# Optimization experiments

Measured on AMD Instinct MI355X. Metric: run time of the kernel, lower is better.

## Reference

```python
import jax, jax.numpy as jnp
import numpy as np

SIGMA_E, SIGMA_I, K_E, K_I = 0.6, 1.2, 0.8, 1.0
PM_STEPS, DT, BETA = 4, 0.15, 1.0
EPS = 1e-4


def setup_inputs() -> dict:
    key = jax.random.key(0)
    ks = jax.random.split(key, 12)
    B, d_in, d_lat, ch, d_out, n_c = 4096, 784, 8, 32, 10, 16
    inp = {
        "x": jax.random.normal(ks[0], (B, d_in), dtype=jnp.float32),
        "W1": jax.random.normal(ks[1], (d_in, 128), dtype=jnp.float32) * 0.03,
        "b1": jnp.zeros((128,), jnp.float32),
        "W2": jax.random.normal(ks[2], (128, d_lat), dtype=jnp.float32) * 0.08,
        "b2": jnp.zeros((d_lat,), jnp.float32),
        "centers": jax.random.normal(ks[3], (n_c, d_lat), dtype=jnp.float32) * 0.7,
        "mus": jnp.ones((n_c,), jnp.float32) * 0.5,
        "Wp": jax.random.normal(ks[4], (d_lat, ch), dtype=jnp.float32) * 0.3,
        "bp": jnp.zeros((ch,), jnp.float32),
        "Wr": jax.random.normal(ks[5], (ch, d_out), dtype=jnp.float32) * 0.15,
        "br": jnp.zeros((d_out,), jnp.float32),
        "T": 5,
    }
    return inp


def grad_ln_n(z, centers, mus):
    # z: [B,d], centers: [C,d], mus: [C]
    rvec = z[:, None, :] - centers[None, :, :]          # [B,C,d]
    r = jnp.sqrt(jnp.sum(rvec * rvec, axis=-1) + EPS)   # [B,C]
    n = 1.0 + jnp.sum(mus[None, :] / r, axis=1)          # [B]
    g = -jnp.sum((mus[None, :] / (r ** 3))[:, :, None] * rvec, axis=1)  # [B,d]
    return g / n[:, None]


def pm_field(z, centers, mus):
    for _ in range(PM_STEPS):
        z = jnp.clip(z + DT * BETA * grad_ln_n(z, centers, mus), -3.0, 3.0)
    return z


def lateral_kernel(z):
    # squared pairwise distances via the norm trick (avoids [B,B,d])
    sq = jnp.sum(z * z, axis=1)
    dist2 = jnp.maximum(sq[:, None] + sq[None, :] - 2.0 * (z @ z.T), 0.0)
    K = K_E * jnp.exp(-dist2 / (2.0 * SIGMA_E ** 2)) - K_I * jnp.exp(-dist2 / (2.0 * SIGMA_I ** 2))
    return jax.lax.stop_gradient(K)  # torch.no_grad in original


def reference(x, W1, b1, W2, b2, centers, mus, Wp, bp, Wr, br, T):
    B = x.shape[0]
    z = jnp.tanh(x.reshape(B, -1) @ W1 + b1) @ W2 + b2   # encoder
    h = jnp.zeros((B, Wr.shape[0]), x.dtype)
    for _ in range(T):
        z = pm_field(z, centers, mus)
        h = 0.9 * h + 0.1 * jnp.tanh(z @ Wp + bp)
        h = h + 0.05 * (lateral_kernel(z) @ h)
        y = h @ Wr + br
    return y
```

## Files before the change

kernel.cpp:

```cpp
#include <hip/hip_runtime.h>
#include <math.h>

#define NB    4096
#define DIN   784
#define DH    128
#define DL    8
#define NC    16
#define NCH   32
#define DO    10
#define TSTEPS 5

#define KH_ROWS   128
#define KH_JSLICE 128
#define KH_P      (NB / KH_JSLICE)
#define ENC_G     7

typedef float v2f __attribute__((ext_vector_type(2)));


__global__ __launch_bounds__(256) void enc1_kernel(const float* __restrict__ x,
    const float* __restrict__ W1, double* __restrict__ P)
{
    __shared__ float xsT[56][18];
    __shared__ float wss[56][128];
    const int tid = threadIdx.x;
    const int m0 = blockIdx.x * 16;
    const int kbeg = blockIdx.y * 112;
    const int cg = tid & 31, rg = tid >> 5;
    const int c0 = cg << 2, r0 = rg << 1;
    double acc[2][4] = {};
    for (int it = 0; it < 2; ++it) {
        const int k0 = kbeg + it * 56;
        __syncthreads();
        if (tid < 224) {
            int row = tid / 14, f = tid % 14;
            float4 v = *(const float4*)(x + (m0 + row) * DIN + k0 + f * 4);
            int kk = f * 4;
            xsT[kk][row] = v.x; xsT[kk + 1][row] = v.y;
            xsT[kk + 2][row] = v.z; xsT[kk + 3][row] = v.w;
        }
        for (int l = tid; l < 56 * 32; l += 256) {
            int kk = l >> 5, c = (l & 31) << 2;
            *(float4*)&wss[kk][c] = *(const float4*)(W1 + (k0 + kk) * DH + c);
        }
        __syncthreads();
#pragma unroll 8
        for (int kk = 0; kk < 56; ++kk) {
            const float2 xv = *(const float2*)&xsT[kk][r0];
            const float4 wv = *(const float4*)&wss[kk][c0];
            const double x0 = (double)xv.x, x1 = (double)xv.y;
            const double w0 = (double)wv.x, w1 = (double)wv.y;
            const double w2v = (double)wv.z, w3 = (double)wv.w;
            acc[0][0] += x0 * w0; acc[0][1] += x0 * w1;
            acc[0][2] += x0 * w2v; acc[0][3] += x0 * w3;
            acc[1][0] += x1 * w0; acc[1][1] += x1 * w1;
            acc[1][2] += x1 * w2v; acc[1][3] += x1 * w3;
        }
    }
    double* Pr = P + (size_t)blockIdx.y * (NB * DH);
#pragma unroll
    for (int i = 0; i < 2; ++i) {
        double* dst = Pr + (m0 + r0 + i) * DH + c0;
        *(double2*)dst       = make_double2(acc[i][0], acc[i][1]);
        *(double2*)(dst + 2) = make_double2(acc[i][2], acc[i][3]);
    }
}

__global__ __launch_bounds__(256) void enc2_kernel(const double* __restrict__ P,
    const float* __restrict__ b1, const float* __restrict__ W2,
    const float* __restrict__ b2, double* __restrict__ zbuf)
{
    __shared__ double As[16][132];
    __shared__ double W2d[DH * DL];
    const int tid = threadIdx.x;
    const int m0 = blockIdx.x * 16;
    for (int l = tid; l < DH * DL; l += 256) W2d[l] = (double)W2[l];
    for (int l = tid; l < 16 * 128; l += 256) {
        int row = l >> 7, k = l & 127;
        double v = (double)b1[k];
#pragma unroll
        for (int s = 0; s < ENC_G; ++s)
            v += P[(size_t)s * NB * DH + (m0 + row) * DH + k];
        As[row][k] = tanh(v);
    }
    __syncthreads();
    const int row = tid >> 4, d = (tid >> 1) & 7, half = tid & 1;
    double a = 0.0;
#pragma unroll 8
    for (int i = 0; i < 64; ++i) {
        const int k = half + (i << 1);
        a += As[row][k] * W2d[k * 8 + d];
    }
    a += __shfl_xor(a, 1);
    if (half == 0) zbuf[(m0 + row) * DL + d] = a + (double)b2[d];
}

__global__ __launch_bounds__(256) void enc_fused_kernel(const float* __restrict__ x,
    const float* __restrict__ W1, const float* __restrict__ b1,
    const float* __restrict__ W2, const float* __restrict__ b2,
    double* __restrict__ zbuf)
{
    __shared__ float  xsT[56][9];
    __shared__ float  wss[56][128];
    __shared__ double Asd[8][131];
    __shared__ double W2d[DH * DL];
    const int tid = threadIdx.x;
    const int m0 = blockIdx.x * 8;
    const int cg = tid & 31, rg = tid >> 5;
    const int c0 = cg << 2;
    for (int l = tid; l < DH * DL; l += 256) W2d[l] = (double)W2[l];
    double acc[4] = {};
    for (int it = 0; it < 14; ++it) {
        const int k0 = it * 56;
        __syncthreads();
        if (tid < 112) {
            int row = tid / 14, f = tid % 14;
            float4 v = *(const float4*)(x + (m0 + row) * DIN + k0 + f * 4);
            int kk = f * 4;
            xsT[kk][row] = v.x; xsT[kk + 1][row] = v.y;
            xsT[kk + 2][row] = v.z; xsT[kk + 3][row] = v.w;
        }
        for (int l = tid; l < 56 * 32; l += 256) {
            int kk = l >> 5, c = (l & 31) << 2;
            *(float4*)&wss[kk][c] = *(const float4*)(W1 + (k0 + kk) * DH + c);
        }
        __syncthreads();
#pragma unroll 8
        for (int kk = 0; kk < 56; ++kk) {
            const double xv = (double)xsT[kk][rg];
            const float4 wv = *(const float4*)&wss[kk][c0];
            acc[0] += xv * (double)wv.x;
            acc[1] += xv * (double)wv.y;
            acc[2] += xv * (double)wv.z;
            acc[3] += xv * (double)wv.w;
        }
    }
    __syncthreads();
#pragma unroll
    for (int j = 0; j < 4; ++j)
        Asd[rg][c0 + j] = tanh(acc[j] + (double)b1[c0 + j]);
    __syncthreads();
    {
        const int row = tid >> 5, d = (tid >> 2) & 7, kq = tid & 3;
        double a = 0.0;
#pragma unroll 8
        for (int i = 0; i < 32; ++i) {
            const int k = kq + (i << 2);
            a += Asd[row][k] * W2d[k * 8 + d];
        }
        a += __shfl_xor(a, 1);
        a += __shfl_xor(a, 2);
        if (kq == 0) zbuf[(m0 + row) * DL + d] = a + (double)b2[d];
    }
}

__global__ __launch_bounds__(64) void pmh_kernel(double* __restrict__ zbuf,
    const float* __restrict__ centers, const float* __restrict__ mus,
    const float* __restrict__ Wp, const float* __restrict__ bp,
    double* __restrict__ hB, float* __restrict__ zf, float* __restrict__ sqf,
    float* __restrict__ hAf, const float* __restrict__ part, int first)
{
    const int tid = threadIdx.x;
    const int lane = tid & 15;
    const int s = tid >> 4;
    const int i = blockIdx.x * 4 + s;
    double cz[8];
#pragma unroll
    for (int d = 0; d < 8; ++d) cz[d] = (double)centers[lane * DL + d];
    const double mu = (double)mus[lane];
    double z[8];
#pragma unroll
    for (int p = 0; p < 4; ++p) {
        double2 v = *(const double2*)(zbuf + i * DL + p * 2);
        z[p * 2] = v.x; z[p * 2 + 1] = v.y;
    }
#pragma unroll
    for (int st = 0; st < 4; ++st) {
        double rv[8];
        double ss = 1e-4;
#pragma unroll
        for (int d = 0; d < 8; ++d) { rv[d] = z[d] - cz[d]; ss += rv[d] * rv[d]; }
        double rinv = rsqrt(ss);
        double mr = mu * rinv;
        double n = mr;
        double mr3 = mr * (rinv * rinv);
        double g[8];
#pragma unroll
        for (int d = 0; d < 8; ++d) g[d] = -mr3 * rv[d];
#pragma unroll
        for (int m = 1; m < 16; m <<= 1) {
            n += __shfl_xor(n, m);
#pragma unroll
            for (int d = 0; d < 8; ++d) g[d] += __shfl_xor(g[d], m);
        }
        double sc = 0.15 / (1.0 + n);
#pragma unroll
        for (int d = 0; d < 8; ++d) z[d] = fmin(3.0, fmax(-3.0, z[d] + sc * g[d]));
    }
    if (lane == 0) {
        double sq = 0.0;
#pragma unroll
        for (int d = 0; d < 8; ++d) sq += z[d] * z[d];
        sqf[i] = (float)sq;
#pragma unroll
        for (int p = 0; p < 4; ++p)
            *(double2*)(zbuf + i * DL + p * 2) = make_double2(z[p * 2], z[p * 2 + 1]);
        float4 a = make_float4((float)z[0], (float)z[1], (float)z[2], (float)z[3]);
        float4 b = make_float4((float)z[4], (float)z[5], (float)z[6], (float)z[7]);
        *(float4*)(zf + i * DL)     = a;
        *(float4*)(zf + i * DL + 4) = b;
    }
#pragma unroll
    for (int cc = 0; cc < 2; ++cc) {
        const int c = lane + cc * 16;
        double a = (double)bp[c];
#pragma unroll
        for (int d = 0; d < 8; ++d) a += z[d] * (double)Wp[d * NCH + c];
        double ph = (double)tanhf((float)a);
        double prev = 0.0;
        if (!first) {
            prev = hB[i * NCH + c];
            if (part) {
                double sp = 0.0;
#pragma unroll
                for (int p = 0; p < KH_P; ++p)
                    sp += (double)part[(size_t)p * (NB * NCH) + i * NCH + c];
                prev += 0.05 * sp;
            }
        }
        double hv = 0.9 * prev + 0.1 * ph;
        hAf[i * NCH + c] = (float)hv;
        hB[i * NCH + c] = hv;
    }
}

#define SM_Z   0
#define SM_SQ  1024
#define SM_H   1152
#define SM_ALL 5248
__global__ __launch_bounds__(256) void kh_kernel(const float* __restrict__ zf,
    const float* __restrict__ sqf, const float* __restrict__ hAf,
    double* __restrict__ hB, float* __restrict__ part)
{
    __shared__ float smem[SM_ALL];
    const int tid = threadIdx.x;
    const int wave = tid >> 6, lane = tid & 63;
    const int row0 = blockIdx.x * KH_ROWS + lane;
    const int j0 = blockIdx.y * KH_JSLICE;
    float zr0[8], zr1[8];
    {
        float4 a = *(const float4*)(zf + row0 * 8);
        float4 b = *(const float4*)(zf + row0 * 8 + 4);
        zr0[0] = a.x; zr0[1] = a.y; zr0[2] = a.z; zr0[3] = a.w;
        zr0[4] = b.x; zr0[5] = b.y; zr0[6] = b.z; zr0[7] = b.w;
        float4 c = *(const float4*)(zf + (row0 + 64) * 8);
        float4 d = *(const float4*)(zf + (row0 + 64) * 8 + 4);
        zr1[0] = c.x; zr1[1] = c.y; zr1[2] = c.z; zr1[3] = c.w;
        zr1[4] = d.x; zr1[5] = d.y; zr1[6] = d.z; zr1[7] = d.w;
    }
    const float sq0 = sqf[row0], sq1 = sqf[row0 + 64];
    const float invI = 1.0f / 2.88f;
    {
        int jj = tid >> 1, p = (tid & 1) << 2;
        *(float4*)&smem[SM_Z + jj * 8 + p] = *(const float4*)(zf + (j0 + jj) * 8 + p);
    }
    if (tid < KH_JSLICE) smem[SM_SQ + tid] = sqf[j0 + tid];
    for (int l = tid; l < KH_JSLICE * 8; l += 256) {
        int jh = l >> 3, p = (l & 7) << 2;
        *(float4*)&smem[SM_H + jh * 32 + p] = *(const float4*)(hAf + (j0 + jh) * NCH + p);
    }
    __syncthreads();
    v2f a0[16], a1[16];
#pragma unroll
    for (int k = 0; k < 16; ++k) { a0[k] = (v2f)(0.f); a1[k] = (v2f)(0.f); }
    const int jjbeg = wave * 32;
#pragma unroll 2
    for (int q = 0; q < 32; ++q) {
        const int jj = jjbeg + q;
        const float4 a = *(const float4*)&smem[SM_Z + jj * 8];
        const float4 b = *(const float4*)&smem[SM_Z + jj * 8 + 4];
        const float sqj = smem[SM_SQ + jj];
        float dot0 = zr0[0] * a.x + zr0[1] * a.y + zr0[2] * a.z + zr0[3] * a.w
                   + zr0[4] * b.x + zr0[5] * b.y + zr0[6] * b.z + zr0[7] * b.w;
        float dot1 = zr1[0] * a.x + zr1[1] * a.y + zr1[2] * a.z + zr1[3] * a.w
                   + zr1[4] * b.x + zr1[5] * b.y + zr1[6] * b.z + zr1[7] * b.w;
        float d20 = fmaxf(sq0 + sqj - 2.0f * dot0, 0.0f);
        float d21 = fmaxf(sq1 + sqj - 2.0f * dot1, 0.0f);
        float e0 = __expf(-d20 * invI), e1 = __expf(-d21 * invI);
        float t0 = e0 * e0, t1 = e1 * e1;
        float K0 = 0.8f * (t0 * t0) - e0;
        float K1 = 0.8f * (t1 * t1) - e1;
        const v2f K0v = {K0, K0}, K1v = {K1, K1};
        const v2f* hrow = (const v2f*)&smem[SM_H + jj * 32];
#pragma unroll
        for (int k = 0; k < 16; k += 2) {
            const v2f h0 = hrow[k], h1 = hrow[k + 1];
            a0[k]     += K0v * h0; a0[k + 1] += K0v * h1;
            a1[k]     += K1v * h0; a1[k + 1] += K1v * h1;
        }
    }
    float* acc0 = (float*)a0;
    float* acc1 = (float*)a1;
    __syncthreads();
    if (wave == 1) {
#pragma unroll
        for (int c = 0; c < 32; ++c) { smem[lane * 33 + c] = acc0[c]; smem[(lane + 64) * 33 + c] = acc1[c]; }
    }
    __syncthreads();
    if (wave == 0) {
#pragma unroll
        for (int c = 0; c < 32; ++c) { acc0[c] += smem[lane * 33 + c]; acc1[c] += smem[(lane + 64) * 33 + c]; }
    }
    __syncthreads();
    if (wave == 3) {
#pragma unroll
        for (int c = 0; c < 32; ++c) { smem[lane * 33 + c] = acc0[c]; smem[(lane + 64) * 33 + c] = acc1[c]; }
    }
    __syncthreads();
    if (wave == 2) {
#pragma unroll
        for (int c = 0; c < 32; ++c) { acc0[c] += smem[lane * 33 + c]; acc1[c] += smem[(lane + 64) * 33 + c]; }
    }
    __syncthreads();
    if (wave == 2) {
#pragma unroll
        for (int c = 0; c < 32; ++c) { smem[lane * 33 + c] = acc0[c]; smem[(lane + 64) * 33 + c] = acc1[c]; }
    }
    __syncthreads();
    if (wave == 0) {
#pragma unroll
        for (int c = 0; c < 32; ++c) { acc0[c] += smem[lane * 33 + c]; acc1[c] += smem[(lane + 64) * 33 + c]; }
        if (part) {
            float* p0 = part + (size_t)blockIdx.y * (NB * NCH) + row0 * NCH;
            float* p1 = p0 + 64 * NCH;
#pragma unroll
            for (int c = 0; c < 32; c += 4) {
                *(float4*)(p0 + c) = make_float4(acc0[c], acc0[c + 1], acc0[c + 2], acc0[c + 3]);
                *(float4*)(p1 + c) = make_float4(acc1[c], acc1[c + 1], acc1[c + 2], acc1[c + 3]);
            }
        } else {
#pragma unroll
            for (int c = 0; c < 32; ++c) {
                atomicAdd(&hB[row0 * NCH + c], 0.05 * (double)acc0[c]);
                atomicAdd(&hB[(row0 + 64) * NCH + c], 0.05 * (double)acc1[c]);
            }
        }
    }
}

__global__ __launch_bounds__(256) void y_kernel(const double* __restrict__ h,
    const float* __restrict__ part, const float* __restrict__ Wr,
    const float* __restrict__ br, float* __restrict__ y)
{
    __shared__ double hsy[16][33];
    __shared__ double wrs[NCH * DO];
    __shared__ double brs[DO];
    const int tid = threadIdx.x;
    const int rb = blockIdx.x * 16;
    for (int l = tid; l < 16 * 32; l += 256) {
        int row = l >> 5, k = l & 31;
        const int gi = (rb + row) * NCH + k;
        double v = h[gi];
        if (part) {
            double sp = 0.0;
#pragma unroll
            for (int p = 0; p < KH_P; ++p) sp += (double)part[(size_t)p * (NB * NCH) + gi];
            v += 0.05 * sp;
        }
        hsy[row][k] = v;
    }
    for (int l = tid; l < NCH * DO; l += 256) wrs[l] = (double)Wr[l];
    if (tid < DO) brs[tid] = (double)br[tid];
    __syncthreads();
    const int row = tid >> 4, col = tid & 15;
    if (col < DO) {
        double a = brs[col];
#pragma unroll
        for (int k = 0; k < NCH; ++k) a += hsy[row][k] * wrs[k * DO + col];
        y[(rb + row) * DO + col] = (float)a;
    }
}

extern "C" void kernel_launch(void* const* d_in, const int* in_sizes, int n_in,
                              void* d_out, int out_size, void* d_ws, size_t ws_size,
                              hipStream_t stream)
{
    const float* x   = (const float*)d_in[0];
    const float* W1  = (const float*)d_in[1];
    const float* b1  = (const float*)d_in[2];
    const float* W2  = (const float*)d_in[3];
    const float* b2  = (const float*)d_in[4];
    const float* cen = (const float*)d_in[5];
    const float* mus = (const float*)d_in[6];
    const float* Wp  = (const float*)d_in[7];
    const float* bp  = (const float*)d_in[8];
    const float* Wr  = (const float*)d_in[9];
    const float* br  = (const float*)d_in[10];

    float* y = (float*)d_out;
    double* zbuf = (double*)d_ws;
    double* hB   = zbuf + NB * DL;
    float*  zf   = (float*)(hB + NB * NCH);
    float*  sqf  = zf + NB * DL;
    float*  hAf  = sqf + NB;
    float*  part = hAf + NB * NCH;
    double* Penc = (double*)(part + (size_t)KH_P * NB * NCH);

    const size_t need_part = (size_t)(NB * DL + NB * NCH) * 8
                           + (size_t)(NB * DL + NB + NB * NCH + KH_P * NB * NCH) * 4;
    const size_t need_full = need_part + (size_t)ENC_G * NB * DH * 8;
    float* pp = (ws_size >= need_part) ? part : (float*)nullptr;

    if (ws_size >= need_full) {
        enc1_kernel<<<dim3(NB / 16, ENC_G), 256, 0, stream>>>(x, W1, Penc);
        enc2_kernel<<<NB / 16, 256, 0, stream>>>(Penc, b1, W2, b2, zbuf);
    } else {
        enc_fused_kernel<<<NB / 8, 256, 0, stream>>>(x, W1, b1, W2, b2, zbuf);
    }
    for (int t = 0; t < TSTEPS; ++t) {
        pmh_kernel<<<NB / 4, 64, 0, stream>>>(zbuf, cen, mus, Wp, bp, hB,
                                              zf, sqf, hAf, pp, t == 0 ? 1 : 0);
        kh_kernel<<<dim3(NB / KH_ROWS, KH_P), 256, 0, stream>>>(zf, sqf, hAf, hB, pp);
    }
    y_kernel<<<NB / 16, 256, 0, stream>>>(hB, pp, Wr, br, y);
}
```

Before: 331.3 us.

## Fuse time-step loop into one persistent cooperative kernel with grid syncs

Replaces the 11 separate launches (pmh and kh kernels per step plus the y kernel) with a single cooperative persistent kernel. Blocks loop over virtual work items and use grid.sync between the PM/h phase and the lateral-kernel phase. This removes per-launch overhead and inter-kernel gaps, at the cost of grid-wide barriers and fewer resident blocks (grid capped at 1024) than the original launch sizes.

Measured after the change: 996.0 us. 3.01x slower.

```diff
diff --git a/kernel.cpp b/kernel.cpp
--- a/kernel.cpp
+++ b/kernel.cpp
@@ -1,4 +1,5 @@
 #include <hip/hip_runtime.h>
+#include <hip/hip_cooperative_groups.h>
 #include <math.h>
 
 #define NB    4096
@@ -154,6 +155,235 @@
     }
 }
 
+#define SM_Z   0
+#define SM_SQ  1024
+#define SM_H   1152
+#define SM_ALL 5248
+__global__ __launch_bounds__(256, 4) void loop_kernel(
+    double* __restrict__ zbuf, const float* __restrict__ cen,
+    const float* __restrict__ mus, const float* __restrict__ Wp,
+    const float* __restrict__ bp, double* __restrict__ hB,
+    float* __restrict__ zf, float* __restrict__ sqf, float* __restrict__ hAf,
+    float* __restrict__ part, const float* __restrict__ Wr,
+    const float* __restrict__ br, float* __restrict__ y)
+{
+    cooperative_groups::grid_group grid = cooperative_groups::this_grid();
+    __shared__ __align__(16) double dsm[2624];
+    float* smem = (float*)dsm;
+    const int tid = threadIdx.x;
+    const int nB = gridDim.x;
+
+    for (int t = 0; t < TSTEPS; ++t) {
+        {
+            const int wv = tid >> 6, wl = tid & 63;
+            const int l16 = wl & 15, sIdx = wl >> 4;
+            const int w = blockIdx.x * 4 + wv;
+            const int nW = nB * 4;
+            for (int g = w; g < NB / 4; g += nW) {
+                const int i = g * 4 + sIdx;
+                double cz[8];
+#pragma unroll
+                for (int d = 0; d < 8; ++d) cz[d] = (double)cen[l16 * DL + d];
+                const double mu = (double)mus[l16];
+                double z[8];
+#pragma unroll
+                for (int p = 0; p < 4; ++p) {
+                    double2 v = *(const double2*)(zbuf + i * DL + p * 2);
+                    z[p * 2] = v.x; z[p * 2 + 1] = v.y;
+                }
+#pragma unroll
+                for (int st = 0; st < 4; ++st) {
+                    double rv[8];
+                    double ss = 1e-4;
+#pragma unroll
+                    for (int d = 0; d < 8; ++d) { rv[d] = z[d] - cz[d]; ss += rv[d] * rv[d]; }
+                    double rinv = rsqrt(ss);
+                    double mr = mu * rinv;
+                    double n = mr;
+                    double mr3 = mr * (rinv * rinv);
+                    double gv[8];
+#pragma unroll
+                    for (int d = 0; d < 8; ++d) gv[d] = -mr3 * rv[d];
+#pragma unroll
+                    for (int m = 1; m < 16; m <<= 1) {
+                        n += __shfl_xor(n, m);
+#pragma unroll
+                        for (int d = 0; d < 8; ++d) gv[d] += __shfl_xor(gv[d], m);
+                    }
+                    double sc = 0.15 / (1.0 + n);
+#pragma unroll
+                    for (int d = 0; d < 8; ++d) z[d] = fmin(3.0, fmax(-3.0, z[d] + sc * gv[d]));
+                }
+                if (l16 == 0) {
+                    double sq = 0.0;
+#pragma unroll
+                    for (int d = 0; d < 8; ++d) sq += z[d] * z[d];
+                    sqf[i] = (float)sq;
+#pragma unroll
+                    for (int p = 0; p < 4; ++p)
+                        *(double2*)(zbuf + i * DL + p * 2) = make_double2(z[p * 2], z[p * 2 + 1]);
+                    float4 a = make_float4((float)z[0], (float)z[1], (float)z[2], (float)z[3]);
+                    float4 b = make_float4((float)z[4], (float)z[5], (float)z[6], (float)z[7]);
+                    *(float4*)(zf + i * DL)     = a;
+                    *(float4*)(zf + i * DL + 4) = b;
+                }
+#pragma unroll
+                for (int cc = 0; cc < 2; ++cc) {
+                    const int c = l16 + cc * 16;
+                    double a = (double)bp[c];
+#pragma unroll
+                    for (int d = 0; d < 8; ++d) a += z[d] * (double)Wp[d * NCH + c];
+                    double ph = (double)tanhf((float)a);
+                    double prev = 0.0;
+                    if (t != 0) {
+                        prev = hB[i * NCH + c];
+                        double sp = 0.0;
+#pragma unroll 8
+                        for (int p = 0; p < KH_P; ++p)
+                            sp += (double)part[(size_t)p * (NB * NCH) + i * NCH + c];
+                        prev += 0.05 * sp;
+                    }
+                    double hv = 0.9 * prev + 0.1 * ph;
+                    hAf[i * NCH + c] = (float)hv;
+                    hB[i * NCH + c] = hv;
+                }
+            }
+        }
+        grid.sync();
+        {
+            const int wave = tid >> 6, lane = tid & 63;
+            for (int vb = blockIdx.x; vb < (NB / KH_ROWS) * KH_P; vb += nB) {
+                const int bx = vb & (NB / KH_ROWS - 1);
+                const int by = vb / (NB / KH_ROWS);
+                __syncthreads();
+                const int row0 = bx * KH_ROWS + lane;
+                const int j0 = by * KH_JSLICE;
+                float zr0[8], zr1[8];
+                {
+                    float4 a = *(const float4*)(zf + row0 * 8);
+                    float4 b = *(const float4*)(zf + row0 * 8 + 4);
+                    zr0[0] = a.x; zr0[1] = a.y; zr0[2] = a.z; zr0[3] = a.w;
+                    zr0[4] = b.x; zr0[5] = b.y; zr0[6] = b.z; zr0[7] = b.w;
+                    float4 c = *(const float4*)(zf + (row0 + 64) * 8);
+                    float4 d = *(const float4*)(zf + (row0 + 64) * 8 + 4);
+                    zr1[0] = c.x; zr1[1] = c.y; zr1[2] = c.z; zr1[3] = c.w;
+                    zr1[4] = d.x; zr1[5] = d.y; zr1[6] = d.z; zr1[7] = d.w;
+                }
+                const float sq0 = sqf[row0], sq1 = sqf[row0 + 64];
+                const float invI = 1.0f / 2.88f;
+                {
+                    int jj = tid >> 1, p = (tid & 1) << 2;
+                    *(float4*)&smem[SM_Z + jj * 8 + p] = *(const float4*)(zf + (j0 + jj) * 8 + p);
+                }
+                if (tid < KH_JSLICE) smem[SM_SQ + tid] = sqf[j0 + tid];
+                for (int l = tid; l < KH_JSLICE * 8; l += 256) {
+                    int jh = l >> 3, p = (l & 7) << 2;
+                    *(float4*)&smem[SM_H + jh * 32 + p] = *(const float4*)(hAf + (j0 + jh) * NCH + p);
+                }
+                __syncthreads();
+                v2f a0[16], a1[16];
+#pragma unroll
+                for (int k = 0; k < 16; ++k) { a0[k] = (v2f)(0.f); a1[k] = (v2f)(0.f); }
+                const int jjbeg = wave * 32;
+#pragma unroll 2
+                for (int q = 0; q < 32; ++q) {
+                    const int jj = jjbeg + q;
+                    const float4 a = *(const float4*)&smem[SM_Z + jj * 8];
+                    const float4 b = *(const float4*)&smem[SM_Z + jj * 8 + 4];
+                    const float sqj = smem[SM_SQ + jj];
+                    float dot0 = zr0[0] * a.x + zr0[1] * a.y + zr0[2] * a.z + zr0[3] * a.w
+                               + zr0[4] * b.x + zr0[5] * b.y + zr0[6] * b.z + zr0[7] * b.w;
+                    float dot1 = zr1[0] * a.x + zr1[1] * a.y + zr1[2] * a.z + zr1[3] * a.w
+                               + zr1[4] * b.x + zr1[5] * b.y + zr1[6] * b.z + zr1[7] * b.w;
+                    float d20 = fmaxf(sq0 + sqj - 2.0f * dot0, 0.0f);
+                    float d21 = fmaxf(sq1 + sqj - 2.0f * dot1, 0.0f);
+                    float e0 = __expf(-d20 * invI), e1 = __expf(-d21 * invI);
+                    float t0 = e0 * e0, t1 = e1 * e1;
+                    float K0 = 0.8f * (t0 * t0) - e0;
+                    float K1 = 0.8f * (t1 * t1) - e1;
+                    const v2f K0v = {K0, K0}, K1v = {K1, K1};
+                    const v2f* hrow = (const v2f*)&smem[SM_H + jj * 32];
+#pragma unroll
+                    for (int k = 0; k < 16; k += 2) {
+                        const v2f h0 = hrow[k], h1 = hrow[k + 1];
+                        a0[k]     += K0v * h0; a0[k + 1] += K0v * h1;
+                        a1[k]     += K1v * h0; a1[k + 1] += K1v * h1;
+                    }
+                }
+                float* acc0 = (float*)a0;
+                float* acc1 = (float*)a1;
+                __syncthreads();
+                if (wave == 1) {
+#pragma unroll
+                    for (int c = 0; c < 32; ++c) { smem[lane * 33 + c] = acc0[c]; smem[(lane + 64) * 33 + c] = acc1[c]; }
+                }
+                __syncthreads();
+                if (wave == 0) {
+#pragma unroll
+                    for (int c = 0; c < 32; ++c) { acc0[c] += smem[lane * 33 + c]; acc1[c] += smem[(lane + 64) * 33 + c]; }
+                }
+                __syncthreads();
+                if (wave == 3) {
+#pragma unroll
+                    for (int c = 0; c < 32; ++c) { smem[lane * 33 + c] = acc0[c]; smem[(lane + 64) * 33 + c] = acc1[c]; }
+                }
+                __syncthreads();
+                if (wave == 2) {
+#pragma unroll
+                    for (int c = 0; c < 32; ++c) { acc0[c] += smem[lane * 33 + c]; acc1[c] += smem[(lane + 64) * 33 + c]; }
+                }
+                __syncthreads();
+                if (wave == 2) {
+#pragma unroll
+                    for (int c = 0; c < 32; ++c) { smem[lane * 33 + c] = acc0[c]; smem[(lane + 64) * 33 + c] = acc1[c]; }
+                }
+                __syncthreads();
+                if (wave == 0) {
+#pragma unroll
+                    for (int c = 0; c < 32; ++c) { acc0[c] += smem[lane * 33 + c]; acc1[c] += smem[(lane + 64) * 33 + c]; }
+                    float* p0 = part + (size_t)by * (NB * NCH) + row0 * NCH;
+                    float* p1 = p0 + 64 * NCH;
+#pragma unroll
+                    for (int c = 0; c < 32; c += 4) {
+                        *(float4*)(p0 + c) = make_float4(acc0[c], acc0[c + 1], acc0[c + 2], acc0[c + 3]);
+                        *(float4*)(p1 + c) = make_float4(acc1[c], acc1[c + 1], acc1[c + 2], acc1[c + 3]);
+                    }
+                }
+            }
+        }
+        grid.sync();
+    }
+    {
+        double* hsy = dsm;
+        double* wrs = dsm + 16 * 33;
+        double* brs = wrs + NCH * DO;
+        for (int vb = blockIdx.x; vb < NB / 16; vb += nB) {
+            const int rb = vb * 16;
+            __syncthreads();
+            for (int l = tid; l < 16 * 32; l += 256) {
+                int row = l >> 5, k = l & 31;
+                const int gi = (rb + row) * NCH + k;
+                double v = hB[gi];
+                double sp = 0.0;
+#pragma unroll 8
+                for (int p = 0; p < KH_P; ++p) sp += (double)part[(size_t)p * (NB * NCH) + gi];
+                v += 0.05 * sp;
+                hsy[row * 33 + k] = v;
+            }
+            for (int l = tid; l < NCH * DO; l += 256) wrs[l] = (double)Wr[l];
+            if (tid < DO) brs[tid] = (double)br[tid];
+            __syncthreads();
+            const int row = tid >> 4, col = tid & 15;
+            if (col < DO) {
+                double a = brs[col];
+#pragma unroll
+                for (int k = 0; k < NCH; ++k) a += hsy[row * 33 + k] * wrs[k * DO + col];
+                y[(rb + row) * DO + col] = (float)a;
+            }
+        }
+    }
+}
+
 __global__ __launch_bounds__(64) void pmh_kernel(double* __restrict__ zbuf,
     const float* __restrict__ centers, const float* __restrict__ mus,
     const float* __restrict__ Wp, const float* __restrict__ bp,
@@ -234,10 +464,6 @@
     }
 }
 
-#define SM_Z   0
-#define SM_SQ  1024
-#define SM_H   1152
-#define SM_ALL 5248
 __global__ __launch_bounds__(256) void kh_kernel(const float* __restrict__ zf,
     const float* __restrict__ sqf, const float* __restrict__ hAf,
     double* __restrict__ hB, float* __restrict__ part)
@@ -409,7 +635,6 @@
     const size_t need_part = (size_t)(NB * DL + NB * NCH) * 8
                            + (size_t)(NB * DL + NB + NB * NCH + KH_P * NB * NCH) * 4;
     const size_t need_full = need_part + (size_t)ENC_G * NB * DH * 8;
-    float* pp = (ws_size >= need_part) ? part : (float*)nullptr;
 
     if (ws_size >= need_full) {
         enc1_kernel<<<dim3(NB / 16, ENC_G), 256, 0, stream>>>(x, W1, Penc);
@@ -417,10 +642,35 @@
     } else {
         enc_fused_kernel<<<NB / 8, 256, 0, stream>>>(x, W1, b1, W2, b2, zbuf);
     }
-    for (int t = 0; t < TSTEPS; ++t) {
-        pmh_kernel<<<NB / 4, 64, 0, stream>>>(zbuf, cen, mus, Wp, bp, hB,
-                                              zf, sqf, hAf, pp, t == 0 ? 1 : 0);
-        kh_kernel<<<dim3(NB / KH_ROWS, KH_P), 256, 0, stream>>>(zf, sqf, hAf, hB, pp);
-    }
-    y_kernel<<<NB / 16, 256, 0, stream>>>(hB, pp, Wr, br, y);
-}
+
+    if (ws_size >= need_part) {
+        static int G = -1;
+        if (G < 0) {
+            int maxb = 0;
+            if (hipOccupancyMaxActiveBlocksPerMultiprocessor(&maxb, loop_kernel, 256, 0)
+                    != hipSuccess || maxb < 1)
+                maxb = 1;
+            int dev = 0, cus = 0;
+            hipGetDevice(&dev);
+            if (hipDeviceGetAttribute(&cus, hipDeviceAttributeMultiprocessorCount, dev)
+                    != hipSuccess || cus <= 0)
+                cus = 256;
+            long cap = (long)maxb * (long)cus;
+            G = (int)(cap < 1024 ? cap : 1024);
+            if (G < 1) G = 1;
+        }
+        void* args[] = { (void*)&zbuf, (void*)&cen, (void*)&mus, (void*)&Wp,
+                         (void*)&bp, (void*)&hB, (void*)&zf, (void*)&sqf,
+                         (void*)&hAf, (void*)&part, (void*)&Wr, (void*)&br,
+                         (void*)&y };
+        hipLaunchCooperativeKernel(loop_kernel, dim3(G), dim3(256), args, 0, stream);
+    } else {
+        float* pp = nullptr;
+        for (int t = 0; t < TSTEPS; ++t) {
+            pmh_kernel<<<NB / 4, 64, 0, stream>>>(zbuf, cen, mus, Wp, bp, hB,
+                                                  zf, sqf, hAf, pp, t == 0 ? 1 : 0);
+            kh_kernel<<<dim3(NB / KH_ROWS, KH_P), 256, 0, stream>>>(zf, sqf, hAf, hB, pp);
+        }
+        y_kernel<<<NB / 16, 256, 0, stream>>>(hB, pp, Wr, br, y);
+    }
+}
```
